# Optimization experiments

Measured on AMD Instinct MI355X. Metric: run time of the kernel, lower is better.

Reference implementation:

```python
import jax, jax.numpy as jnp
import numpy as np

L, N, E, D_MODEL, H = 3, 50000, 600000, 128, 8
D = D_MODEL // H          # per-head dim = 16
DFF = 4 * D_MODEL         # feedforward hidden = 512


def prelu(x, a):
    return jnp.where(x >= 0, x, a * x)


def layernorm(x, scale, bias, eps=1e-5):
    m = x.mean(-1, keepdims=True)
    v = x.var(-1, keepdims=True)
    return (x - m) * jax.lax.rsqrt(v + eps) * scale + bias


def setup_inputs() -> dict:
    key = jax.random.key(0)
    ks = jax.random.split(key, 16)
    s = 1.0 / np.sqrt(D_MODEL)
    return {
        "in_feats": jax.random.normal(ks[0], (N, D_MODEL), jnp.float32),
        "src": jax.random.randint(ks[1], (E,), 0, N, jnp.int32),
        "dst": jax.random.randint(ks[2], (E,), 0, N, jnp.int32),
        # per-layer stacked parameters
        "W": jax.random.normal(ks[3], (L, D_MODEL, D_MODEL), jnp.float32) * s,
        "attn_l": jax.random.normal(ks[4], (L, H, D), jnp.float32) * s,
        "attn_r": jax.random.normal(ks[5], (L, H, D), jnp.float32) * s,
        "conv_bias": jnp.zeros((L, H, D), jnp.float32),
        "a_conv": jnp.full((L,), 0.25, jnp.float32),   # PReLU slope after conv
        "ln_scale": jnp.ones((L, D_MODEL), jnp.float32),
        "ln_bias": jnp.zeros((L, D_MODEL), jnp.float32),
        "W1": jax.random.normal(ks[6], (L, D_MODEL, DFF), jnp.float32) * s,
        "b1": jnp.zeros((L, DFF), jnp.float32),
        "W2": jax.random.normal(ks[7], (L, DFF, D_MODEL), jnp.float32) / np.sqrt(DFF),
        "b2": jnp.zeros((L, D_MODEL), jnp.float32),
        "a_ff": jnp.full((L,), 0.25, jnp.float32),     # PReLU slope in FF
    }


def _gat_conv(x, src, dst, W, attn_l, attn_r, conv_bias, a_conv):
    # DGL GATConv: project, per-edge additive attention, edge-softmax over dst, scatter.
    z = (x @ W).reshape(N, H, D)                    # [N,H,D]
    el = (z * attn_l).sum(-1)                       # [N,H]
    er = (z * attn_r).sum(-1)                       # [N,H]
    e = jax.nn.leaky_relu(el[src] + er[dst], 0.2)   # [E,H]
    emax = jax.ops.segment_max(e, dst, num_segments=N)
    emax = jnp.where(jnp.isfinite(emax), emax, 0.0)  # zero in-degree guard
    ex = jnp.exp(e - emax[dst])                     # [E,H]
    denom = jax.ops.segment_sum(ex, dst, num_segments=N)  # [N,H]
    msg = ex[:, :, None] * z[src]                   # [E,H,D]
    agg = jax.ops.segment_sum(msg, dst, num_segments=N)   # [N,H,D]
    out = agg / jnp.maximum(denom, 1e-9)[:, :, None]
    out = prelu(out + conv_bias, a_conv)            # bias + PReLU activation
    return out.reshape(N, H * D)


def reference(in_feats, src, dst, W, attn_l, attn_r, conv_bias, a_conv,
              ln_scale, ln_bias, W1, b1, W2, b2, a_ff):
    outputs = []
    x = in_feats
    for l in range(L):
        h = _gat_conv(x, src, dst, W[l], attn_l[l], attn_r[l], conv_bias[l], a_conv[l])
        h = layernorm(h, ln_scale[l], ln_bias[l])   # layer['norm']
        # FeedForward, norm_first=True, sharing the same LayerNorm params
        hn = layernorm(h, ln_scale[l], ln_bias[l])
        ff = prelu(hn @ W1[l] + b1[l], a_ff[l]) @ W2[l] + b2[l]
        x = h + ff
        outputs.append(x)
    return jnp.stack(outputs)                       # [L, N, d]
```

## Files before the change

kernel.cpp:

```cpp
#include <hip/hip_runtime.h>

#define DM 128
#define NH 8
#define DFF 512

typedef __attribute__((ext_vector_type(8))) short bf16x8;
typedef __attribute__((ext_vector_type(4))) float f32x4;

__device__ __forceinline__ short f2bf(float f) {
    union { float f; unsigned u; } v; v.f = f;
    unsigned r = v.u + 0x7fffu + ((v.u >> 16) & 1u);
    return (short)(r >> 16);
}
__device__ __forceinline__ float bf2f(unsigned short b) {
    union { unsigned u; float f; } v; v.u = ((unsigned)b) << 16; return v.f;
}

template<int ROWS>
__device__ __forceinline__ void stage_tile(
    const short* __restrict__ g, int row0, int maxrow, int rstride, int kbase,
    short* s, int tid)
{
    const int wave = tid >> 6, lane = tid & 63;
#pragma unroll
    for (int rr = 0; rr < ROWS / 16; ++rr) {
        int idx = rr * 256 + wave * 64 + lane;
        int row = idx >> 4, kc = idx & 15;
        int rg = row0 + row;
        rg = (rg < maxrow) ? rg : (maxrow - 1);
        const short* src = g + (size_t)rg * rstride + kbase
                         + ((kc ^ (row & 15)) << 3);
        short* dst = s + (size_t)(rr * 256 + wave * 64) * 8;
        __builtin_amdgcn_global_load_lds(
            (const __attribute__((address_space(1))) void*)src,
            (__attribute__((address_space(3))) void*)dst, 16, 0, 0);
    }
}

__device__ __forceinline__ bf16x8 frag_ld(const short* s, int row, int ks, int g)
{
    return *(const bf16x8*)(s + row * 128 + ((((ks << 2) + g) ^ (row & 15)) << 3));
}

template<bool PRELU, int BM, int NOUT>
__global__ __launch_bounds__(256) void gemm_stage(
    const short* __restrict__ A, const short* __restrict__ Bt,
    const float* __restrict__ bias, const float* __restrict__ affp,
    int M, short* __restrict__ outbf)
{
    __shared__ __align__(16) short sA[BM * 128];
    __shared__ __align__(16) short sB[128 * 128];
    constexpr int IM = BM / 32;

    const int tid = threadIdx.x;
    const int wave = tid >> 6, lane = tid & 63;
    const int wm = wave >> 1, wn = wave & 1;
    const int bm = blockIdx.y * BM, bn = blockIdx.x * 128;
    const int row0w = wm * (BM / 2);

    stage_tile<BM>(A, bm, M, 128, 0, sA, tid);
    stage_tile<128>(Bt + (size_t)bn * 128, 0, 128, 128, 0, sB, tid);
    __syncthreads();

    const int fr = lane & 15, g = lane >> 4;
    f32x4 acc[IM][4];
#pragma unroll
    for (int i = 0; i < IM; ++i)
#pragma unroll
        for (int j = 0; j < 4; ++j) acc[i][j] = (f32x4)0.0f;

#pragma unroll
    for (int ks = 0; ks < 4; ++ks) {
        bf16x8 af[IM], bv[4];
#pragma unroll
        for (int i = 0; i < IM; ++i) af[i] = frag_ld(sA, row0w + i * 16 + fr, ks, g);
#pragma unroll
        for (int j = 0; j < 4; ++j) bv[j] = frag_ld(sB, wn * 64 + j * 16 + fr, ks, g);
#pragma unroll
        for (int i = 0; i < IM; ++i)
#pragma unroll
            for (int j = 0; j < 4; ++j)
                acc[i][j] = __builtin_amdgcn_mfma_f32_16x16x32_bf16(
                    af[i], bv[j], acc[i][j], 0, 0, 0);
    }

    const int lr4 = (lane >> 4) << 2, lc = lane & 15;
    float aff = 0.0f;
    if constexpr (PRELU) aff = *affp;
#pragma unroll
    for (int i = 0; i < IM; ++i)
#pragma unroll
        for (int j = 0; j < 4; ++j) {
            int colL = wn * 64 + j * 16 + lc;
            float bb = 0.0f;
            if constexpr (PRELU) bb = bias[bn + colL];
#pragma unroll
            for (int r = 0; r < 4; ++r) {
                int row = bm + row0w + i * 16 + lr4 + r;
                if (row >= M) continue;
                float v = acc[i][j][r];
                if constexpr (PRELU) {
                    v += bb;
                    v = (v >= 0.0f) ? v : aff * v;
                }
                outbf[(size_t)row * NOUT + bn + colL] = f2bf(v);
            }
        }
}

__global__ __launch_bounds__(256) void ffn2_gemm(
    const short* __restrict__ H1, const short* __restrict__ W2t,
    const short* __restrict__ h_bf, const float* __restrict__ b2,
    int M, float* __restrict__ xo, short* __restrict__ xbf)
{
    __shared__ __align__(16) short sA[64 * 128];
    __shared__ __align__(16) short sB[128 * 128];

    const int tid = threadIdx.x;
    const int wave = tid >> 6, lane = tid & 63;
    const int wm = wave >> 1, wn = wave & 1;
    const int bm = blockIdx.x * 64;
    const int fr = lane & 15, g = lane >> 4;

    f32x4 acc[2][4];
#pragma unroll
    for (int i = 0; i < 2; ++i)
#pragma unroll
        for (int j = 0; j < 4; ++j) acc[i][j] = (f32x4)0.0f;

    for (int c = 0; c < 4; ++c) {
        if (c) __syncthreads();
        stage_tile<64>(H1, bm, M, DFF, c * 128, sA, tid);
        stage_tile<128>(W2t, 0, 128, DFF, c * 128, sB, tid);
        __syncthreads();
#pragma unroll
        for (int ks = 0; ks < 4; ++ks) {
            bf16x8 af[2], bv[4];
#pragma unroll
            for (int i = 0; i < 2; ++i) af[i] = frag_ld(sA, wm * 32 + i * 16 + fr, ks, g);
#pragma unroll
            for (int j = 0; j < 4; ++j) bv[j] = frag_ld(sB, wn * 64 + j * 16 + fr, ks, g);
#pragma unroll
            for (int i = 0; i < 2; ++i)
#pragma unroll
                for (int j = 0; j < 4; ++j)
                    acc[i][j] = __builtin_amdgcn_mfma_f32_16x16x32_bf16(
                        af[i], bv[j], acc[i][j], 0, 0, 0);
        }
    }

    const int lr4 = (lane >> 4) << 2, lc = lane & 15;
#pragma unroll
    for (int i = 0; i < 2; ++i)
#pragma unroll
        for (int j = 0; j < 4; ++j) {
            int colL = wn * 64 + j * 16 + lc;
            float bb = b2[colL];
#pragma unroll
            for (int r = 0; r < 4; ++r) {
                int row = bm + wm * 32 + i * 16 + lr4 + r;
                int rc = (row < M) ? row : (M - 1);
                float v = acc[i][j][r] + bb
                        + bf2f((unsigned short)h_bf[(size_t)rc * DM + colL]);
                if (row < M) {
                    xo[(size_t)row * DM + colL]  = v;
                    xbf[(size_t)row * DM + colL] = f2bf(v);
                }
            }
        }
}

__global__ void wt_conv_kernel(const float* __restrict__ in, short* __restrict__ out,
                               int R, int C, int nL)
{
    int idx = blockIdx.x * blockDim.x + threadIdx.x;
    if (idx >= nL * R * C) return;
    int l = idx / (R * C);
    int rem = idx - l * (R * C);
    int r = rem / C, c = rem - r * C;
    out[(size_t)l * R * C + (size_t)c * R + r] = f2bf(in[idx]);
}

__global__ void f2bf_kernel(const float* __restrict__ in, short* __restrict__ out, int n)
{
    int idx = blockIdx.x * blockDim.x + threadIdx.x;
    if (idx < n) out[idx] = f2bf(in[idx]);
}

__global__ void el_er_kernel(const short* __restrict__ z,
                             const float* __restrict__ al,
                             const float* __restrict__ ar,
                             float* __restrict__ el, float* __restrict__ er, int N)
{
    int idx = blockIdx.x * blockDim.x + threadIdx.x;
    if (idx >= N * NH) return;
    int n = idx >> 3, h = idx & 7;
    const unsigned* zp = (const unsigned*)(z + (size_t)n * DM + h * 16);
    const float* alp = al + h * 16;
    const float* arp = ar + h * 16;
    float sl = 0.0f, sr = 0.0f;
#pragma unroll
    for (int d2 = 0; d2 < 8; ++d2) {
        unsigned u = zp[d2];
        float z0 = bf2f((unsigned short)(u & 0xffff));
        float z1 = bf2f((unsigned short)(u >> 16));
        sl = fmaf(z0, alp[2 * d2], sl);     sl = fmaf(z1, alp[2 * d2 + 1], sl);
        sr = fmaf(z0, arp[2 * d2], sr);     sr = fmaf(z1, arp[2 * d2 + 1], sr);
    }
    el[idx] = sl;
    er[idx] = sr;
}

__global__ void hist_kernel(const int* __restrict__ dst, int* __restrict__ deg, int E)
{
    int e = blockIdx.x * blockDim.x + threadIdx.x;
    if (e < E) atomicAdd(&deg[dst[e]], 1);
}

__global__ void scan1_kernel(const int* __restrict__ deg, int* __restrict__ incl,
                             int* __restrict__ bsum, int N)
{
    __shared__ int sm[256];
    int i = blockIdx.x * 256 + threadIdx.x;
    int v = (i < N) ? deg[i] : 0;
    sm[threadIdx.x] = v;
    __syncthreads();
    for (int off = 1; off < 256; off <<= 1) {
        int t = (threadIdx.x >= off) ? sm[threadIdx.x - off] : 0;
        __syncthreads();
        sm[threadIdx.x] += t;
        __syncthreads();
    }
    if (i < N) incl[i] = sm[threadIdx.x];
    if (threadIdx.x == 255) bsum[blockIdx.x] = sm[255];
}

__global__ void scan2_kernel(int* __restrict__ bsum, int nb)
{
    __shared__ int sm[256];
    int v = (threadIdx.x < nb) ? bsum[threadIdx.x] : 0;
    sm[threadIdx.x] = v;
    __syncthreads();
    for (int off = 1; off < 256; off <<= 1) {
        int t = (threadIdx.x >= off) ? sm[threadIdx.x - off] : 0;
        __syncthreads();
        sm[threadIdx.x] += t;
        __syncthreads();
    }
    if (threadIdx.x < nb) bsum[threadIdx.x] = sm[threadIdx.x];
}

__global__ void scan3_kernel(const int* __restrict__ incl, const int* __restrict__ bsum,
                             int* __restrict__ row_ptr, int N)
{
    int i = blockIdx.x * 256 + threadIdx.x;
    if (i < N) {
        int off = (blockIdx.x > 0) ? bsum[blockIdx.x - 1] : 0;
        row_ptr[i + 1] = incl[i] + off;
    }
    if (i == 0) row_ptr[0] = 0;
}

__global__ void scatter_kernel(const int* __restrict__ src, const int* __restrict__ dst,
                               const int* __restrict__ row_ptr, int* __restrict__ cursor,
                               int* __restrict__ csr_src, int E)
{
    int e = blockIdx.x * blockDim.x + threadIdx.x;
    if (e >= E) return;
    int t = dst[e];
    int pos = atomicAdd(&cursor[t], 1);
    csr_src[row_ptr[t] + pos] = src[e];
}

__global__ __launch_bounds__(256) void gat_agg_ln_kernel(
    const int* __restrict__ row_ptr, const int* __restrict__ csr_src,
    const short* __restrict__ z, const float* __restrict__ el,
    const float* __restrict__ er, const float* __restrict__ cb,
    const float* __restrict__ a_conv,
    const float* __restrict__ scale, const float* __restrict__ bias,
    short* __restrict__ h_out, short* __restrict__ hn_out, int N)
{
    int wave = threadIdx.x >> 6, lane = threadIdx.x & 63;
    int t = blockIdx.x * 4 + wave;
    if (t >= N) return;
    int h = lane >> 3;
    int c0 = 2 * lane, c1 = c0 + 1;
    float er_t = er[t * NH + h];
    int e0 = row_ptr[t], e1 = row_ptr[t + 1];
    float acc0 = 0.0f, acc1 = 0.0f, den = 0.0f;
    const unsigned* zw = (const unsigned*)z;

    int e = e0;
    for (; e + 8 <= e1; e += 8) {
        int s[8];
#pragma unroll
        for (int k = 0; k < 8; ++k) s[k] = csr_src[e + k];
        float x[8]; unsigned u[8];
#pragma unroll
        for (int k = 0; k < 8; ++k) x[k] = el[s[k] * NH + h];
#pragma unroll
        for (int k = 0; k < 8; ++k) u[k] = zw[(size_t)s[k] * 64 + lane];
#pragma unroll
        for (int k = 0; k < 8; ++k) {
            float v = x[k] + er_t;
            v = (v >= 0.0f) ? v : 0.2f * v;
            float w = __expf(v);
            den += w;
            acc0 = fmaf(w, bf2f((unsigned short)(u[k] & 0xffff)), acc0);
            acc1 = fmaf(w, bf2f((unsigned short)(u[k] >> 16)),   acc1);
        }
    }
    for (; e + 4 <= e1; e += 4) {
        int s[4];
#pragma unroll
        for (int k = 0; k < 4; ++k) s[k] = csr_src[e + k];
        float x[4]; unsigned u[4];
#pragma unroll
        for (int k = 0; k < 4; ++k) x[k] = el[s[k] * NH + h];
#pragma unroll
        for (int k = 0; k < 4; ++k) u[k] = zw[(size_t)s[k] * 64 + lane];
#pragma unroll
        for (int k = 0; k < 4; ++k) {
            float v = x[k] + er_t;
            v = (v >= 0.0f) ? v : 0.2f * v;
            float w = __expf(v);
            den += w;
            acc0 = fmaf(w, bf2f((unsigned short)(u[k] & 0xffff)), acc0);
            acc1 = fmaf(w, bf2f((unsigned short)(u[k] >> 16)),   acc1);
        }
    }
    for (; e < e1; ++e) {
        int s = csr_src[e];
        float v = el[s * NH + h] + er_t;
        v = (v >= 0.0f) ? v : 0.2f * v;
        float w = __expf(v);
        den += w;
        unsigned u = zw[(size_t)s * 64 + lane];
        acc0 = fmaf(w, bf2f((unsigned short)(u & 0xffff)), acc0);
        acc1 = fmaf(w, bf2f((unsigned short)(u >> 16)), acc1);
    }

    float a = *a_conv;
    float inv = 1.0f / fmaxf(den, 1e-9f);
    float o0 = acc0 * inv + cb[c0];
    float o1 = acc1 * inv + cb[c1];
    o0 = (o0 >= 0.0f) ? o0 : a * o0;
    o1 = (o1 >= 0.0f) ? o1 : a * o1;

    float sc0 = scale[c0], sc1 = scale[c1];
    float bi0 = bias[c0], bi1 = bias[c1];

    float s1 = o0 + o1, ss = o0 * o0 + o1 * o1;
#pragma unroll
    for (int off = 32; off > 0; off >>= 1) {
        s1 += __shfl_xor(s1, off, 64);
        ss += __shfl_xor(ss, off, 64);
    }
    float mean = s1 * (1.0f / 128.0f);
    float var = ss * (1.0f / 128.0f) - mean * mean;
    float rstd = rsqrtf(var + 1e-5f);
    float h0 = (o0 - mean) * rstd * sc0 + bi0;
    float h1 = (o1 - mean) * rstd * sc1 + bi1;
    unsigned hlo = (unsigned short)f2bf(h0);
    unsigned hhi = (unsigned short)f2bf(h1);
    ((unsigned*)h_out)[(size_t)t * 64 + lane] = hlo | (hhi << 16);

    s1 = h0 + h1; ss = h0 * h0 + h1 * h1;
#pragma unroll
    for (int off = 32; off > 0; off >>= 1) {
        s1 += __shfl_xor(s1, off, 64);
        ss += __shfl_xor(ss, off, 64);
    }
    mean = s1 * (1.0f / 128.0f);
    var = ss * (1.0f / 128.0f) - mean * mean;
    rstd = rsqrtf(var + 1e-5f);
    unsigned lo = (unsigned short)f2bf((h0 - mean) * rstd * sc0 + bi0);
    unsigned hi = (unsigned short)f2bf((h1 - mean) * rstd * sc1 + bi1);
    ((unsigned*)hn_out)[(size_t)t * 64 + lane] = lo | (hi << 16);
}

extern "C" void kernel_launch(void* const* d_in, const int* in_sizes, int n_in,
                              void* d_out, int out_size, void* d_ws, size_t ws_size,
                              hipStream_t stream)
{
    const float* in_feats = (const float*)d_in[0];
    const int*   src      = (const int*)d_in[1];
    const int*   dst      = (const int*)d_in[2];
    const float* W        = (const float*)d_in[3];
    const float* attn_l   = (const float*)d_in[4];
    const float* attn_r   = (const float*)d_in[5];
    const float* convb    = (const float*)d_in[6];
    const float* a_conv   = (const float*)d_in[7];
    const float* ln_scale = (const float*)d_in[8];
    const float* ln_bias  = (const float*)d_in[9];
    const float* W1       = (const float*)d_in[10];
    const float* b1       = (const float*)d_in[11];
    const float* W2       = (const float*)d_in[12];
    const float* b2       = (const float*)d_in[13];
    const float* a_ff     = (const float*)d_in[14];
    float* out = (float*)d_out;

    const int N = in_sizes[0] / DM;
    const int E = in_sizes[1];
    const int L = in_sizes[7];

    char* wsb = (char*)d_ws;
    size_t off = 0;
    auto alloc = [&](size_t bytes) { char* p = wsb + off; off += (bytes + 255) & ~(size_t)255; return p; };

    short* z_bf  = (short*)alloc((size_t)N * DM * sizeof(short));
    short* h_bf  = (short*)alloc((size_t)N * DM * sizeof(short));
    short* hn_bf = (short*)alloc((size_t)N * DM * sizeof(short));
    short* x_bf  = (short*)alloc((size_t)N * DM * sizeof(short));
    short* H1    = (short*)alloc((size_t)N * DFF * sizeof(short));
    float* el    = (float*)alloc((size_t)N * NH * sizeof(float));
    float* er    = (float*)alloc((size_t)N * NH * sizeof(float));
    short* Wt    = (short*)alloc((size_t)L * DM * DM * sizeof(short));
    short* W1t   = (short*)alloc((size_t)L * DFF * DM * sizeof(short));
    short* W2t   = (short*)alloc((size_t)L * DM * DFF * sizeof(short));
    int* deg     = (int*)alloc((size_t)N * sizeof(int));
    int* incl    = (int*)alloc((size_t)N * sizeof(int));
    int* bsum    = (int*)alloc(256 * sizeof(int));
    int* row_ptr = (int*)alloc((size_t)(N + 1) * sizeof(int));
    int* cursor  = (int*)alloc((size_t)N * sizeof(int));
    int* csr_src = (int*)alloc((size_t)E * sizeof(int));

    const int gM128 = (N + 127) / 128;
    const int gM64  = (N + 63) / 64;
    const int nbScan = (N + 255) / 256;

    hipMemsetAsync(deg, 0, (size_t)N * sizeof(int), stream);
    hipMemsetAsync(cursor, 0, (size_t)N * sizeof(int), stream);
    hist_kernel<<<(E + 255) / 256, 256, 0, stream>>>(dst, deg, E);
    scan1_kernel<<<nbScan, 256, 0, stream>>>(deg, incl, bsum, N);
    scan2_kernel<<<1, 256, 0, stream>>>(bsum, nbScan);
    scan3_kernel<<<nbScan, 256, 0, stream>>>(incl, bsum, row_ptr, N);
    scatter_kernel<<<(E + 255) / 256, 256, 0, stream>>>(src, dst, row_ptr, cursor, csr_src, E);

    wt_conv_kernel<<<(L * DM * DM + 255) / 256, 256, 0, stream>>>(W, Wt, DM, DM, L);
    wt_conv_kernel<<<(L * DM * DFF + 255) / 256, 256, 0, stream>>>(W1, W1t, DM, DFF, L);
    wt_conv_kernel<<<(L * DFF * DM + 255) / 256, 256, 0, stream>>>(W2, W2t, DFF, DM, L);
    f2bf_kernel<<<(N * DM + 255) / 256, 256, 0, stream>>>(in_feats, x_bf, N * DM);

    gemm_stage<false, 64, DM><<<dim3(1, gM64), 256, 0, stream>>>(
        x_bf, Wt, nullptr, nullptr, N, z_bf);

    for (int l = 0; l < L; ++l) {
        float* xo = out + (size_t)l * N * DM;

        el_er_kernel<<<(N * NH + 255) / 256, 256, 0, stream>>>(
            z_bf, attn_l + (size_t)l * NH * 16, attn_r + (size_t)l * NH * 16, el, er, N);

        gat_agg_ln_kernel<<<(N + 3) / 4, 256, 0, stream>>>(
            row_ptr, csr_src, z_bf, el, er, convb + (size_t)l * DM, a_conv + l,
            ln_scale + (size_t)l * DM, ln_bias + (size_t)l * DM, h_bf, hn_bf, N);

        gemm_stage<true, 128, DFF><<<dim3(4, gM128), 256, 0, stream>>>(
            hn_bf, W1t + (size_t)l * DFF * DM, b1 + (size_t)l * DFF, a_ff + l, N, H1);

        ffn2_gemm<<<gM64, 256, 0, stream>>>(
            H1, W2t + (size_t)l * DM * DFF, h_bf, b2 + (size_t)l * DM, N, xo, x_bf);

        if (l + 1 < L)
            gemm_stage<false, 64, DM><<<dim3(1, gM64), 256, 0, stream>>>(
                x_bf, Wt + (size_t)(l + 1) * DM * DM, nullptr, nullptr, N, z_bf);
    }
}
```

Measured before the change: 563.0 us.

## Pipeline bf16 GEMMs with triple-buffered async LDS staging and persistent tiles

Replaces the one-tile-per-block GEMMs with a persistent 512-thread kernel. Each block loads its weight tile into LDS once, then streams 64-row A tiles through a triple buffer using async global-to-LDS loads and explicit vmcnt waits. The FFN2 GEMM is likewise rebuilt to triple-buffer its four K-chunks, so the next chunk loads while the current one is multiplied. The aim is to hide load latency and avoid reloading weights, at the cost of fragile hand-counted waits that assume a fixed number of outstanding stores per tile, and a larger LDS footprint.

```diff
diff --git a/kernel.cpp b/kernel.cpp
--- a/kernel.cpp
+++ b/kernel.cpp
@@ -6,6 +6,9 @@
 
 typedef __attribute__((ext_vector_type(8))) short bf16x8;
 typedef __attribute__((ext_vector_type(4))) float f32x4;
+
+#define WAITVM(N) do { asm volatile("s_waitcnt vmcnt(" #N ")" ::: "memory"); \
+                       __builtin_amdgcn_sched_barrier(0); } while (0)
 
 __device__ __forceinline__ short f2bf(float f) {
     union { float f; unsigned u; } v; v.f = f;
@@ -16,21 +19,21 @@
     union { unsigned u; float f; } v; v.u = ((unsigned)b) << 16; return v.f;
 }
 
-template<int ROWS>
+template<int ROWS, int NT>
 __device__ __forceinline__ void stage_tile(
     const short* __restrict__ g, int row0, int maxrow, int rstride, int kbase,
     short* s, int tid)
 {
-    const int wave = tid >> 6, lane = tid & 63;
-#pragma unroll
-    for (int rr = 0; rr < ROWS / 16; ++rr) {
-        int idx = rr * 256 + wave * 64 + lane;
+    const int lane = tid & 63;
+#pragma unroll
+    for (int rr = 0; rr < ROWS * 16 / NT; ++rr) {
+        int idx = rr * NT + tid;
         int row = idx >> 4, kc = idx & 15;
         int rg = row0 + row;
         rg = (rg < maxrow) ? rg : (maxrow - 1);
         const short* src = g + (size_t)rg * rstride + kbase
                          + ((kc ^ (row & 15)) << 3);
-        short* dst = s + (size_t)(rr * 256 + wave * 64) * 8;
+        short* dst = s + (size_t)(idx - lane) * 8;
         __builtin_amdgcn_global_load_lds(
             (const __attribute__((address_space(1))) void*)src,
             (__attribute__((address_space(3))) void*)dst, 16, 0, 0);
@@ -42,132 +45,143 @@
     return *(const bf16x8*)(s + row * 128 + ((((ks << 2) + g) ^ (row & 15)) << 3));
 }
 
-template<bool PRELU, int BM, int NOUT>
-__global__ __launch_bounds__(256) void gemm_stage(
+template<bool PRELU, int NOUT>
+__global__ __launch_bounds__(512, 4) void gemm_k128_stream(
     const short* __restrict__ A, const short* __restrict__ Bt,
     const float* __restrict__ bias, const float* __restrict__ affp,
     int M, short* __restrict__ outbf)
 {
-    __shared__ __align__(16) short sA[BM * 128];
-    __shared__ __align__(16) short sB[128 * 128];
-    constexpr int IM = BM / 32;
+    __shared__ __align__(16) short sW[128 * 128];
+    __shared__ __align__(16) short sA[3][64 * 128];
 
     const int tid = threadIdx.x;
     const int wave = tid >> 6, lane = tid & 63;
     const int wm = wave >> 1, wn = wave & 1;
-    const int bm = blockIdx.y * BM, bn = blockIdx.x * 128;
-    const int row0w = wm * (BM / 2);
-
-    stage_tile<BM>(A, bm, M, 128, 0, sA, tid);
-    stage_tile<128>(Bt + (size_t)bn * 128, 0, 128, 128, 0, sB, tid);
-    __syncthreads();
-
+    const int bn = blockIdx.x * 128;
     const int fr = lane & 15, g = lane >> 4;
-    f32x4 acc[IM][4];
-#pragma unroll
-    for (int i = 0; i < IM; ++i)
-#pragma unroll
-        for (int j = 0; j < 4; ++j) acc[i][j] = (f32x4)0.0f;
-
-#pragma unroll
-    for (int ks = 0; ks < 4; ++ks) {
-        bf16x8 af[IM], bv[4];
-#pragma unroll
-        for (int i = 0; i < IM; ++i) af[i] = frag_ld(sA, row0w + i * 16 + fr, ks, g);
-#pragma unroll
-        for (int j = 0; j < 4; ++j) bv[j] = frag_ld(sB, wn * 64 + j * 16 + fr, ks, g);
-#pragma unroll
-        for (int i = 0; i < IM; ++i)
-#pragma unroll
-            for (int j = 0; j < 4; ++j)
-                acc[i][j] = __builtin_amdgcn_mfma_f32_16x16x32_bf16(
-                    af[i], bv[j], acc[i][j], 0, 0, 0);
-    }
-
-    const int lr4 = (lane >> 4) << 2, lc = lane & 15;
-    float aff = 0.0f;
-    if constexpr (PRELU) aff = *affp;
-#pragma unroll
-    for (int i = 0; i < IM; ++i)
-#pragma unroll
-        for (int j = 0; j < 4; ++j) {
-            int colL = wn * 64 + j * 16 + lc;
-            float bb = 0.0f;
-            if constexpr (PRELU) bb = bias[bn + colL];
+    const int lr4 = g << 2, lc = fr;
+    const int nT = (M + 63) >> 6;
+    const int GY = gridDim.y;
+    const int t0 = blockIdx.y;
+    const int nLoc = (t0 < nT) ? ((nT - 1 - t0) / GY + 1) : 0;
+
+    float bb[4]; float aff = 0.0f;
+    if constexpr (PRELU) {
+        aff = *affp;
+#pragma unroll
+        for (int cg = 0; cg < 4; ++cg)
+            bb[cg] = bias[bn + wn * 64 + cg * 16 + lc];
+    }
+
+    stage_tile<128, 512>(Bt + (size_t)bn * 128, 0, 128, 128, 0, sW, tid);
+    if (nLoc > 0) stage_tile<64, 512>(A, t0 * 64, M, 128, 0, sA[0], tid);
+    if (nLoc > 1) stage_tile<64, 512>(A, (t0 + GY) * 64, M, 128, 0, sA[1], tid);
+
+    for (int i = 0; i < nLoc; ++i) {
+        const int t = t0 + i * GY;
+        if (i >= 1 && i + 1 < nLoc)
+            stage_tile<64, 512>(A, (t + GY) * 64, M, 128, 0, sA[(i + 1) % 3], tid);
+
+        if (i == 0) { if (nLoc > 1) WAITVM(2); else WAITVM(0); }
+        else WAITVM(16);
+        __builtin_amdgcn_s_barrier();
+
+        const short* sAb = sA[i % 3];
+        f32x4 acc[4];
+#pragma unroll
+        for (int cg = 0; cg < 4; ++cg) acc[cg] = (f32x4)0.0f;
+
+#pragma unroll
+        for (int ks = 0; ks < 4; ++ks) {
+            bf16x8 af = frag_ld(sAb, wm * 16 + fr, ks, g);
+#pragma unroll
+            for (int cg = 0; cg < 4; ++cg) {
+                bf16x8 bf = frag_ld(sW, wn * 64 + cg * 16 + fr, ks, g);
+                acc[cg] = __builtin_amdgcn_mfma_f32_16x16x32_bf16(
+                    af, bf, acc[cg], 0, 0, 0);
+            }
+        }
+
+#pragma unroll
+        for (int cg = 0; cg < 4; ++cg) {
+            int colL = wn * 64 + cg * 16 + lc;
 #pragma unroll
             for (int r = 0; r < 4; ++r) {
-                int row = bm + row0w + i * 16 + lr4 + r;
-                if (row >= M) continue;
-                float v = acc[i][j][r];
-                if constexpr (PRELU) {
-                    v += bb;
-                    v = (v >= 0.0f) ? v : aff * v;
+                int row = t * 64 + wm * 16 + lr4 + r;
+                if (row < M) {
+                    float v = acc[cg][r];
+                    if constexpr (PRELU) {
+                        v += bb[cg];
+                        v = (v >= 0.0f) ? v : aff * v;
+                    }
+                    outbf[(size_t)row * NOUT + bn + colL] = f2bf(v);
                 }
-                outbf[(size_t)row * NOUT + bn + colL] = f2bf(v);
             }
         }
-}
-
-__global__ __launch_bounds__(256) void ffn2_gemm(
+    }
+}
+
+__global__ __launch_bounds__(512) void ffn2_pipe(
     const short* __restrict__ H1, const short* __restrict__ W2t,
     const short* __restrict__ h_bf, const float* __restrict__ b2,
     int M, float* __restrict__ xo, short* __restrict__ xbf)
 {
-    __shared__ __align__(16) short sA[64 * 128];
-    __shared__ __align__(16) short sB[128 * 128];
+    __shared__ __align__(16) short sA[3][64 * 128];
+    __shared__ __align__(16) short sB[3][128 * 128];
 
     const int tid = threadIdx.x;
     const int wave = tid >> 6, lane = tid & 63;
     const int wm = wave >> 1, wn = wave & 1;
     const int bm = blockIdx.x * 64;
     const int fr = lane & 15, g = lane >> 4;
-
-    f32x4 acc[2][4];
-#pragma unroll
-    for (int i = 0; i < 2; ++i)
-#pragma unroll
-        for (int j = 0; j < 4; ++j) acc[i][j] = (f32x4)0.0f;
-
+    const int lr4 = g << 2, lc = fr;
+
+    f32x4 acc[4];
+#pragma unroll
+    for (int cg = 0; cg < 4; ++cg) acc[cg] = (f32x4)0.0f;
+
+    stage_tile<64, 512>(H1, bm, M, DFF, 0, sA[0], tid);
+    stage_tile<128, 512>(W2t, 0, 128, DFF, 0, sB[0], tid);
+
+#pragma unroll
     for (int c = 0; c < 4; ++c) {
-        if (c) __syncthreads();
-        stage_tile<64>(H1, bm, M, DFF, c * 128, sA, tid);
-        stage_tile<128>(W2t, 0, 128, DFF, c * 128, sB, tid);
-        __syncthreads();
+        if (c < 3) {
+            stage_tile<64, 512>(H1, bm, M, DFF, (c + 1) * 128, sA[(c + 1) % 3], tid);
+            stage_tile<128, 512>(W2t, 0, 128, DFF, (c + 1) * 128, sB[(c + 1) % 3], tid);
+        }
+        if (c < 3) WAITVM(6); else WAITVM(0);
+        __builtin_amdgcn_s_barrier();
+
+        const short* a = sA[c % 3];
+        const short* b = sB[c % 3];
 #pragma unroll
         for (int ks = 0; ks < 4; ++ks) {
-            bf16x8 af[2], bv[4];
-#pragma unroll
-            for (int i = 0; i < 2; ++i) af[i] = frag_ld(sA, wm * 32 + i * 16 + fr, ks, g);
-#pragma unroll
-            for (int j = 0; j < 4; ++j) bv[j] = frag_ld(sB, wn * 64 + j * 16 + fr, ks, g);
-#pragma unroll
-            for (int i = 0; i < 2; ++i)
-#pragma unroll
-                for (int j = 0; j < 4; ++j)
-                    acc[i][j] = __builtin_amdgcn_mfma_f32_16x16x32_bf16(
-                        af[i], bv[j], acc[i][j], 0, 0, 0);
-        }
-    }
-
-    const int lr4 = (lane >> 4) << 2, lc = lane & 15;
-#pragma unroll
-    for (int i = 0; i < 2; ++i)
-#pragma unroll
-        for (int j = 0; j < 4; ++j) {
-            int colL = wn * 64 + j * 16 + lc;
-            float bb = b2[colL];
-#pragma unroll
-            for (int r = 0; r < 4; ++r) {
-                int row = bm + wm * 32 + i * 16 + lr4 + r;
-                int rc = (row < M) ? row : (M - 1);
-                float v = acc[i][j][r] + bb
-                        + bf2f((unsigned short)h_bf[(size_t)rc * DM + colL]);
-                if (row < M) {
-                    xo[(size_t)row * DM + colL]  = v;
-                    xbf[(size_t)row * DM + colL] = f2bf(v);
-                }
+            bf16x8 af = frag_ld(a, wm * 16 + fr, ks, g);
+#pragma unroll
+            for (int cg = 0; cg < 4; ++cg) {
+                bf16x8 bf = frag_ld(b, wn * 64 + cg * 16 + fr, ks, g);
+                acc[cg] = __builtin_amdgcn_mfma_f32_16x16x32_bf16(
+                    af, bf, acc[cg], 0, 0, 0);
             }
         }
+    }
+
+#pragma unroll
+    for (int cg = 0; cg < 4; ++cg) {
+        int colL = wn * 64 + cg * 16 + lc;
+        float bbv = b2[colL];
+#pragma unroll
+        for (int r = 0; r < 4; ++r) {
+            int row = bm + wm * 16 + lr4 + r;
+            int rc = (row < M) ? row : (M - 1);
+            float v = acc[cg][r] + bbv
+                    + bf2f((unsigned short)h_bf[(size_t)rc * DM + colL]);
+            if (row < M) {
+                xo[(size_t)row * DM + colL]  = v;
+                xbf[(size_t)row * DM + colL] = f2bf(v);
+            }
+        }
+    }
 }
 
 __global__ void wt_conv_kernel(const float* __restrict__ in, short* __restrict__ out,
@@ -425,7 +439,6 @@
     int* cursor  = (int*)alloc((size_t)N * sizeof(int));
     int* csr_src = (int*)alloc((size_t)E * sizeof(int));
 
-    const int gM128 = (N + 127) / 128;
     const int gM64  = (N + 63) / 64;
     const int nbScan = (N + 255) / 256;
 
@@ -442,7 +455,7 @@
     wt_conv_kernel<<<(L * DFF * DM + 255) / 256, 256, 0, stream>>>(W2, W2t, DFF, DM, L);
     f2bf_kernel<<<(N * DM + 255) / 256, 256, 0, stream>>>(in_feats, x_bf, N * DM);
 
-    gemm_stage<false, 64, DM><<<dim3(1, gM64), 256, 0, stream>>>(
+    gemm_k128_stream<false, DM><<<dim3(1, 512), 512, 0, stream>>>(
         x_bf, Wt, nullptr, nullptr, N, z_bf);
 
     for (int l = 0; l < L; ++l) {
@@ -455,14 +468,14 @@
             row_ptr, csr_src, z_bf, el, er, convb + (size_t)l * DM, a_conv + l,
             ln_scale + (size_t)l * DM, ln_bias + (size_t)l * DM, h_bf, hn_bf, N);
 
-        gemm_stage<true, 128, DFF><<<dim3(4, gM128), 256, 0, stream>>>(
+        gemm_k128_stream<true, DFF><<<dim3(4, 128), 512, 0, stream>>>(
             hn_bf, W1t + (size_t)l * DFF * DM, b1 + (size_t)l * DFF, a_ff + l, N, H1);
 
-        ffn2_gemm<<<gM64, 256, 0, stream>>>(
+        ffn2_pipe<<<gM64, 512, 0, stream>>>(
             H1, W2t + (size_t)l * DM * DFF, h_bf, b2 + (size_t)l * DM, N, xo, x_bf);
 
         if (l + 1 < L)
-            gemm_stage<false, 64, DM><<<dim3(1, gM64), 256, 0, stream>>>(
+            gemm_k128_stream<false, DM><<<dim3(1, 512), 512, 0, stream>>>(
                 x_bf, Wt + (size_t)(l + 1) * DM * DM, nullptr, nullptr, N, z_bf);
     }
 }
```

Result: faster. 506.3 us (-10.1%).
